# Performance work log

Hardware: AMD Instinct MI355X
Metric: run time of the kernel (lower is better)

Reference implementation:

```python
import jax, jax.numpy as jnp
import numpy as np

N = 65536      # points
C = 256        # channels
K = 16         # knn_samples
L = 4          # num_blocks
EXP = 4        # MLP expansion
EPS = 1e-5


def layer_norm(x, g, b):
    m = jnp.mean(x, axis=-1, keepdims=True)
    v = jnp.var(x, axis=-1, keepdims=True)
    return (x - m) * jax.lax.rsqrt(v + EPS) * g + b


def setup_inputs() -> dict:
    key = jax.random.key(0)
    ks = jax.random.split(key, 16)
    s = lambda fan_in: 1.0 / np.sqrt(fan_in)
    inp = {
        "x": jax.random.normal(ks[0], (N, C), jnp.float32),
        "knn_idx": jax.random.randint(ks[1], (N, K), 0, N, jnp.int32),
        # per-block stacked params (PyTorch Linear stored as [in, out] here)
        "ln1_g": jnp.ones((L, C), jnp.float32),
        "ln1_b": jnp.zeros((L, C), jnp.float32),
        "w_qkv": jax.random.uniform(ks[2], (L, C, 3 * C), jnp.float32, -s(C), s(C)),
        "w_proj": jax.random.uniform(ks[3], (L, C, C), jnp.float32, -s(C), s(C)),
        "b_proj": jax.random.uniform(ks[4], (L, C), jnp.float32, -s(C), s(C)),
        "ln2_g": jnp.ones((L, C), jnp.float32),
        "ln2_b": jnp.zeros((L, C), jnp.float32),
        "w_fc1": jax.random.uniform(ks[5], (L, C, EXP * C), jnp.float32, -s(C), s(C)),
        "b_fc1": jax.random.uniform(ks[6], (L, EXP * C), jnp.float32, -s(C), s(C)),
        "w_fc2": jax.random.uniform(ks[7], (L, EXP * C, C), jnp.float32, -s(EXP * C), s(EXP * C)),
        "b_fc2": jax.random.uniform(ks[8], (L, C), jnp.float32, -s(EXP * C), s(EXP * C)),
    }
    return inp


def reference(x, knn_idx, ln1_g, ln1_b, w_qkv, w_proj, b_proj,
              ln2_g, ln2_b, w_fc1, b_fc1, w_fc2, b_fc2):
    scale = C ** (-0.5)  # head_dim == C (num_heads == 1)
    for i in range(L):
        # --- KNN attention ---
        h = layer_norm(x, ln1_g[i], ln1_b[i])
        qkv = h @ w_qkv[i]                       # [N, 3C], no bias
        q, k, v = jnp.split(qkv, 3, axis=-1)     # each [N, C]
        kk = k[knn_idx]                          # [N, K, C] neighbor gather
        vv = v[knn_idx]                          # [N, K, C]
        scores = jnp.einsum('nc,nkc->nk', q, kk) * scale
        attn = jax.nn.softmax(scores, axis=-1)   # softmax over K neighbors
        out = jnp.einsum('nk,nkc->nc', attn, vv)
        x = x + (out @ w_proj[i] + b_proj[i])
        # --- MLP ---
        h2 = layer_norm(x, ln2_g[i], ln2_b[i])
        h2 = jax.nn.gelu(h2 @ w_fc1[i] + b_fc1[i], approximate=False)
        x = x + (h2 @ w_fc2[i] + b_fc2[i])
    return x
```

## Files before the change

### kernel.cpp

```cpp
#include <hip/hip_runtime.h>

typedef __attribute__((ext_vector_type(4))) float  f32x4;
typedef __attribute__((ext_vector_type(2))) float  f32x2;
typedef __attribute__((ext_vector_type(8))) __bf16 bf16x8;
typedef __attribute__((ext_vector_type(4))) short  s16x4;
typedef __attribute__((ext_vector_type(8))) short  s16x8;
typedef unsigned char uchar;

__device__ __forceinline__ unsigned short f2bf(float f) {
  unsigned u = __builtin_bit_cast(unsigned, f);
  u += 0x7FFFu + ((u >> 16) & 1u);
  return (unsigned short)(u >> 16);
}
__device__ __forceinline__ float b2f(short s) {
  return __builtin_bit_cast(float, (unsigned)((unsigned short)s) << 16);
}
__device__ __forceinline__ float gelu_sig(float v) {
  float t = __expf(-1.702f * v);
  return v * __builtin_amdgcn_rcpf(1.f + t);
}

__device__ __forceinline__ void gload16(const void* g, void* l) {
  __builtin_amdgcn_global_load_lds(
      (const __attribute__((address_space(1))) void*)g,
      (__attribute__((address_space(3))) void*)l, 16, 0, 0);
}

__global__ __launch_bounds__(256) void x2bf(const float* __restrict__ x,
                                            short* __restrict__ xb) {
  int i = blockIdx.x * 256 + threadIdx.x;
  float4 v = *(const float4*)(x + (size_t)i * 4);
  s16x4 o;
  o[0] = (short)f2bf(v.x);
  o[1] = (short)f2bf(v.y);
  o[2] = (short)f2bf(v.z);
  o[3] = (short)f2bf(v.w);
  *(s16x4*)(xb + (size_t)i * 4) = o;
}

__global__ __launch_bounds__(256) void wcast(const float* __restrict__ W,
                                             short* __restrict__ WT,
                                             int In, int Out) {
  int i = blockIdx.x * 256 + threadIdx.x;
  int lay = blockIdx.y;
  if (i >= In * Out) return;
  const float* w = W + (size_t)lay * In * Out;
  short* wt = WT + (size_t)lay * In * Out;
  int ii = i % In, oo = i / In;
  wt[(size_t)oo * In + ii] = (short)f2bf(w[(size_t)ii * Out + oo]);
}

__global__ __launch_bounds__(256) void ln_k(const short* __restrict__ xb,
                                            const float* __restrict__ g,
                                            const float* __restrict__ b,
                                            short* __restrict__ out) {
  int row = blockIdx.x * 4 + (threadIdx.x >> 6);
  int l = threadIdx.x & 63;
  const s16x4 vb = *(const s16x4*)(xb + (size_t)row * 256 + l * 4);
  float v0 = b2f(vb[0]), v1 = b2f(vb[1]), v2 = b2f(vb[2]), v3 = b2f(vb[3]);
  float s  = v0 + v1 + v2 + v3;
  float ss = v0 * v0 + v1 * v1 + v2 * v2 + v3 * v3;
#pragma unroll
  for (int o = 32; o >= 1; o >>= 1) {
    s  += __shfl_xor(s, o);
    ss += __shfl_xor(ss, o);
  }
  float mean = s * (1.0f / 256.0f);
  float var  = ss * (1.0f / 256.0f) - mean * mean;
  float rstd = rsqrtf(var + 1e-5f);
  const float4 gg = *(const float4*)(g + l * 4);
  const float4 bb = *(const float4*)(b + l * 4);
  s16x4 o4;
  o4[0] = (short)f2bf((v0 - mean) * rstd * gg.x + bb.x);
  o4[1] = (short)f2bf((v1 - mean) * rstd * gg.y + bb.y);
  o4[2] = (short)f2bf((v2 - mean) * rstd * gg.z + bb.z);
  o4[3] = (short)f2bf((v3 - mean) * rstd * gg.w + bb.w);
  *(s16x4*)(out + (size_t)row * 256 + l * 4) = o4;
}

__global__ __launch_bounds__(256) void attn_k(const short* __restrict__ q_,
                                              const uchar* __restrict__ k8,
                                              const uchar* __restrict__ v8,
                                              const int* __restrict__ knn,
                                              short* __restrict__ out) {
  int n = blockIdx.x * 4 + (threadIdx.x >> 6);
  int l = threadIdx.x & 63;
  int j = l & 15, g = l >> 4;
  int idxj = knn[(size_t)n * 16 + j];
  const short* qp = q_ + (size_t)n * 256 + g * 64;
  const uchar* kp = k8 + (size_t)idxj * 256 + g * 64;
  float partial = 0.f;
#pragma unroll
  for (int t = 0; t < 4; ++t) {
    int4 kv = *(const int4*)(kp + t * 16);
    s16x8 q0 = *(const s16x8*)(qp + t * 16);
    s16x8 q1 = *(const s16x8*)(qp + t * 16 + 8);
    f32x2 a;
    a = __builtin_amdgcn_cvt_pk_f32_fp8(kv.x, false);
    partial += a[0] * b2f(q0[0]) + a[1] * b2f(q0[1]);
    a = __builtin_amdgcn_cvt_pk_f32_fp8(kv.x, true);
    partial += a[0] * b2f(q0[2]) + a[1] * b2f(q0[3]);
    a = __builtin_amdgcn_cvt_pk_f32_fp8(kv.y, false);
    partial += a[0] * b2f(q0[4]) + a[1] * b2f(q0[5]);
    a = __builtin_amdgcn_cvt_pk_f32_fp8(kv.y, true);
    partial += a[0] * b2f(q0[6]) + a[1] * b2f(q0[7]);
    a = __builtin_amdgcn_cvt_pk_f32_fp8(kv.z, false);
    partial += a[0] * b2f(q1[0]) + a[1] * b2f(q1[1]);
    a = __builtin_amdgcn_cvt_pk_f32_fp8(kv.z, true);
    partial += a[0] * b2f(q1[2]) + a[1] * b2f(q1[3]);
    a = __builtin_amdgcn_cvt_pk_f32_fp8(kv.w, false);
    partial += a[0] * b2f(q1[4]) + a[1] * b2f(q1[5]);
    a = __builtin_amdgcn_cvt_pk_f32_fp8(kv.w, true);
    partial += a[0] * b2f(q1[6]) + a[1] * b2f(q1[7]);
  }
  partial += __shfl_xor(partial, 16);
  partial += __shfl_xor(partial, 32);
  float score = partial * 0.0625f;
  float mx = score;
#pragma unroll
  for (int o = 1; o < 16; o <<= 1) mx = fmaxf(mx, __shfl_xor(mx, o));
  float e = __expf(score - mx);
  float sum = e;
#pragma unroll
  for (int o = 1; o < 16; o <<= 1) sum += __shfl_xor(sum, o);
  float attn = e / sum;
  float4 o4 = {0.f, 0.f, 0.f, 0.f};
#pragma unroll
  for (int jj = 0; jj < 16; ++jj) {
    float aj = __shfl(attn, jj);
    int   ij = __shfl(idxj, jj);
    int vv = *(const int*)(v8 + (size_t)ij * 256 + l * 4);
    f32x2 lo = __builtin_amdgcn_cvt_pk_f32_fp8(vv, false);
    f32x2 hi = __builtin_amdgcn_cvt_pk_f32_fp8(vv, true);
    o4.x += aj * lo[0];
    o4.y += aj * lo[1];
    o4.z += aj * hi[0];
    o4.w += aj * hi[1];
  }
  s16x4 ob;
  ob[0] = (short)f2bf(o4.x);
  ob[1] = (short)f2bf(o4.y);
  ob[2] = (short)f2bf(o4.z);
  ob[3] = (short)f2bf(o4.w);
  *(s16x4*)(out + (size_t)n * 256 + l * 4) = ob;
}

template <int EPI, int KD>
__global__ __launch_bounds__(256) void gemm_k(
    const short* __restrict__ A, const short* __restrict__ BT,
    const float* __restrict__ bias, const short* __restrict__ residb,
    short* __restrict__ outb, float* __restrict__ outf,
    uchar* __restrict__ k8, uchar* __restrict__ v8, int Nout, int gx) {
  __shared__ __align__(16) char pool[36864];
  short* lA = (short*)pool;
  short* lB = (short*)(pool + 16384);
  const int tid = threadIdx.x;
  const int l = tid & 63, w = tid >> 6;
  const int nwg = gridDim.x;
  const int bid = blockIdx.x;
  const int swz = (bid & 7) * (nwg >> 3) + (bid >> 3);
  const int m0 = (swz / gx) << 7, n0 = (swz % gx) << 7;
  const int wm = w >> 1, wn = w & 1;

  f32x4 acc[4][4];
#pragma unroll
  for (int i = 0; i < 4; ++i)
#pragma unroll
    for (int jj = 0; jj < 4; ++jj) acc[i][jj] = f32x4{0.f, 0.f, 0.f, 0.f};

  const int srow = (w << 3) + (l >> 3);
  const int scol = (((l & 7) << 3)) ^ ((srow & 7) << 3);
  const short* gA = A + (size_t)(m0 + srow) * KD + scol;
  const short* gB = BT + (size_t)(n0 + srow) * KD + scol;

  for (int kt = 0; kt < KD; kt += 64) {
#pragma unroll
    for (int it = 0; it < 4; ++it) {
      gload16(gA + (size_t)(it * 32) * KD + kt, &lA[(it * 32 + w * 8) * 64]);
      gload16(gB + (size_t)(it * 32) * KD + kt, &lB[(it * 32 + w * 8) * 64]);
    }
    __syncthreads();
#pragma unroll
    for (int kc = 0; kc < 2; ++kc) {
      bf16x8 aF[4], bF[4];
#pragma unroll
      for (int f = 0; f < 4; ++f) {
        int r = wm * 64 + f * 16 + (l & 15);
        int ce = (kc * 32 + ((l >> 4) << 3)) ^ ((r & 7) << 3);
        aF[f] = *(const bf16x8*)(lA + r * 64 + ce);
      }
#pragma unroll
      for (int f = 0; f < 4; ++f) {
        int r = wn * 64 + f * 16 + (l & 15);
        int ce = (kc * 32 + ((l >> 4) << 3)) ^ ((r & 7) << 3);
        bF[f] = *(const bf16x8*)(lB + r * 64 + ce);
      }
#pragma unroll
      for (int mf = 0; mf < 4; ++mf)
#pragma unroll
        for (int nf = 0; nf < 4; ++nf)
          acc[mf][nf] = __builtin_amdgcn_mfma_f32_16x16x32_bf16(
              aF[mf], bF[nf], acc[mf][nf], 0, 0, 0);
    }
    __syncthreads();
  }

  const int lr = (l >> 4) << 2, lc = l & 15;
  if (EPI == 1 || EPI == 4) {
#pragma unroll
    for (int mf = 0; mf < 4; ++mf) {
#pragma unroll
      for (int nf = 0; nf < 4; ++nf) {
#pragma unroll
        for (int jj = 0; jj < 4; ++jj) {
          int row = m0 + wm * 64 + mf * 16 + lr + jj;
          int col = n0 + wn * 64 + nf * 16 + lc;
          float v = acc[mf][nf][jj] + bias[col] +
                    b2f(residb[(size_t)row * 256 + col]);
          if (EPI == 1)
            outb[(size_t)row * 256 + col] = (short)f2bf(v);
          else
            outf[(size_t)row * 256 + col] = v;
        }
      }
    }
    return;
  }

  short* myL = (short*)(pool + w * 9216);
#pragma unroll
  for (int mf = 0; mf < 4; ++mf) {
#pragma unroll
    for (int nf = 0; nf < 4; ++nf) {
#pragma unroll
      for (int jj = 0; jj < 4; ++jj) {
        int rl = mf * 16 + lr + jj;
        int cl = nf * 16 + lc;
        float v = acc[mf][nf][jj];
        if (EPI == 2) v = gelu_sig(v + bias[n0 + wn * 64 + cl]);
        myL[rl * 72 + cl] = (short)f2bf(v);
      }
    }
  }
#pragma unroll
  for (int it = 0; it < 8; ++it) {
    int rl = it * 8 + (l >> 3);
    int cl = (l & 7) * 8;
    s16x8 vv = *(const s16x8*)(myL + rl * 72 + cl);
    int rowg = m0 + wm * 64 + rl;
    int colg = n0 + wn * 64 + cl;
    if (EPI == 2) {
      *(s16x8*)(outb + (size_t)rowg * Nout + colg) = vv;
    } else {
      if (colg < 256) {
        *(s16x8*)(outb + (size_t)rowg * 256 + colg) = vv;
      } else {
        unsigned w0 = __builtin_amdgcn_cvt_pk_fp8_f32(b2f(vv[0]), b2f(vv[1]), 0, false);
        w0 = __builtin_amdgcn_cvt_pk_fp8_f32(b2f(vv[2]), b2f(vv[3]), w0, true);
        unsigned w1 = __builtin_amdgcn_cvt_pk_fp8_f32(b2f(vv[4]), b2f(vv[5]), 0, false);
        w1 = __builtin_amdgcn_cvt_pk_fp8_f32(b2f(vv[6]), b2f(vv[7]), w1, true);
        int2 pk = make_int2((int)w0, (int)w1);
        uchar* dst = (colg < 512) ? (k8 + (size_t)rowg * 256 + (colg - 256))
                                  : (v8 + (size_t)rowg * 256 + (colg - 512));
        *(int2*)dst = pk;
      }
    }
  }
}

extern "C" void kernel_launch(void* const* d_in, const int* in_sizes, int n_in,
                              void* d_out, int out_size, void* d_ws, size_t ws_size,
                              hipStream_t stream) {
  const float* in_x   = (const float*)d_in[0];
  const int*   knn    = (const int*)d_in[1];
  const float* ln1_g  = (const float*)d_in[2];
  const float* ln1_b  = (const float*)d_in[3];
  const float* w_qkv  = (const float*)d_in[4];
  const float* w_proj = (const float*)d_in[5];
  const float* b_proj = (const float*)d_in[6];
  const float* ln2_g  = (const float*)d_in[7];
  const float* ln2_b  = (const float*)d_in[8];
  const float* w_fc1  = (const float*)d_in[9];
  const float* b_fc1  = (const float*)d_in[10];
  const float* w_fc2  = (const float*)d_in[11];
  const float* b_fc2  = (const float*)d_in[12];

  char* ws = (char*)d_ws;
  short* xb   = (short*)(ws);
  short* act  = (short*)(ws + 33554432);
  short* big  = (short*)(ws + 67108864);
  short* q_bf = big;
  uchar* k8   = (uchar*)(ws + 100663296);
  uchar* v8   = (uchar*)(ws + 117440512);
  short* wT   = (short*)(ws + 201326592);
  short* wqkvT  = wT;
  short* wprojT = wT + 786432;
  short* wfc1T  = wT + 1048576;
  short* wfc2T  = wT + 2097152;

  x2bf<<<16384, 256, 0, stream>>>(in_x, xb);
  wcast<<<dim3(768, 4), 256, 0, stream>>>(w_qkv, wqkvT, 256, 768);
  wcast<<<dim3(256, 4), 256, 0, stream>>>(w_proj, wprojT, 256, 256);
  wcast<<<dim3(1024, 4), 256, 0, stream>>>(w_fc1, wfc1T, 256, 1024);
  wcast<<<dim3(1024, 4), 256, 0, stream>>>(w_fc2, wfc2T, 1024, 256);

  for (int i = 0; i < 4; ++i) {
    ln_k<<<16384, 256, 0, stream>>>(xb, ln1_g + i * 256, ln1_b + i * 256, act);
    gemm_k<3, 256><<<3072, 256, 0, stream>>>(
        act, wqkvT + (size_t)i * 196608, nullptr, nullptr, q_bf, nullptr,
        k8, v8, 768, 6);
    attn_k<<<16384, 256, 0, stream>>>(q_bf, k8, v8, knn, act);
    gemm_k<1, 256><<<1024, 256, 0, stream>>>(
        act, wprojT + (size_t)i * 65536, b_proj + i * 256, xb, xb,
        nullptr, nullptr, nullptr, 256, 2);
    ln_k<<<16384, 256, 0, stream>>>(xb, ln2_g + i * 256, ln2_b + i * 256, act);
    gemm_k<2, 256><<<4096, 256, 0, stream>>>(
        act, wfc1T + (size_t)i * 262144, b_fc1 + i * 1024, nullptr, big,
        nullptr, nullptr, nullptr, 1024, 8);
    if (i < 3)
      gemm_k<1, 1024><<<1024, 256, 0, stream>>>(
          big, wfc2T + (size_t)i * 262144, b_fc2 + i * 256, xb, xb,
          nullptr, nullptr, nullptr, 256, 2);
    else
      gemm_k<4, 1024><<<1024, 256, 0, stream>>>(
          big, wfc2T + (size_t)i * 262144, b_fc2 + i * 256, xb, nullptr,
          (float*)d_out, nullptr, nullptr, 256, 2);
  }
}
```

Before: 1.084 ms.

## Fuse LayerNorm into proj and fc2 GEMM epilogues with full-row tiles

Adds a gemm_ln kernel where each 512-thread workgroup computes a 128x256 tile covering the full channel width. It adds bias and residual, writes the bf16 residual stream, then reduces row sum and sum of squares across waves in shared memory to apply the next LayerNorm. This removes seven of the eight standalone ln_k launches and their extra read and write of the activation. The cost is fewer, larger workgroups (512 instead of 1024) and no double buffering in the new kernel. Variance now comes from E[x^2]-mean^2 on the bf16-rounded-before values rather than a separate pass.

```diff
diff --git a/kernel.cpp b/kernel.cpp
--- a/kernel.cpp
+++ b/kernel.cpp
@@ -206,7 +206,7 @@
   }
 
   const int lr = (l >> 4) << 2, lc = l & 15;
-  if (EPI == 1 || EPI == 4) {
+  if (EPI == 4) {
 #pragma unroll
     for (int mf = 0; mf < 4; ++mf) {
 #pragma unroll
@@ -217,10 +217,7 @@
           int col = n0 + wn * 64 + nf * 16 + lc;
           float v = acc[mf][nf][jj] + bias[col] +
                     b2f(residb[(size_t)row * 256 + col]);
-          if (EPI == 1)
-            outb[(size_t)row * 256 + col] = (short)f2bf(v);
-          else
-            outf[(size_t)row * 256 + col] = v;
+          outf[(size_t)row * 256 + col] = v;
         }
       }
     }
@@ -268,6 +265,118 @@
   }
 }
 
+template <int KD>
+__global__ __launch_bounds__(512) void gemm_ln(
+    const short* __restrict__ A, const short* __restrict__ BT,
+    const float* __restrict__ bias, const short* __restrict__ residb,
+    short* __restrict__ xbout, const float* __restrict__ lng,
+    const float* __restrict__ lnb, short* __restrict__ actout) {
+  __shared__ __align__(16) short lA[128 * 64];
+  __shared__ __align__(16) short lB[256 * 64];
+  __shared__ float psum[4][128], psq[4][128];
+  const int tid = threadIdx.x;
+  const int l = tid & 63, w = tid >> 6;
+  const int nwg = gridDim.x;
+  const int bid = blockIdx.x;
+  const int swz = (bid & 7) * (nwg >> 3) + (bid >> 3);
+  const int m0 = swz << 7;
+  const int wm = w >> 2, wn = w & 3;
+
+  f32x4 acc[4][4];
+#pragma unroll
+  for (int i = 0; i < 4; ++i)
+#pragma unroll
+    for (int jj = 0; jj < 4; ++jj) acc[i][jj] = f32x4{0.f, 0.f, 0.f, 0.f};
+
+  const int srow = (w << 3) + (l >> 3);
+  const int scol = (((l & 7) << 3)) ^ ((srow & 7) << 3);
+  const short* gA = A + (size_t)(m0 + srow) * KD + scol;
+  const short* gB = BT + (size_t)srow * KD + scol;
+
+  for (int kt = 0; kt < KD; kt += 64) {
+#pragma unroll
+    for (int it = 0; it < 2; ++it)
+      gload16(gA + (size_t)(it * 64) * KD + kt, &lA[(it * 64 + w * 8) * 64]);
+#pragma unroll
+    for (int it = 0; it < 4; ++it)
+      gload16(gB + (size_t)(it * 64) * KD + kt, &lB[(it * 64 + w * 8) * 64]);
+    __syncthreads();
+#pragma unroll
+    for (int kc = 0; kc < 2; ++kc) {
+      bf16x8 aF[4], bF[4];
+#pragma unroll
+      for (int f = 0; f < 4; ++f) {
+        int r = wm * 64 + f * 16 + (l & 15);
+        int ce = (kc * 32 + ((l >> 4) << 3)) ^ ((r & 7) << 3);
+        aF[f] = *(const bf16x8*)(lA + r * 64 + ce);
+      }
+#pragma unroll
+      for (int f = 0; f < 4; ++f) {
+        int r = wn * 64 + f * 16 + (l & 15);
+        int ce = (kc * 32 + ((l >> 4) << 3)) ^ ((r & 7) << 3);
+        bF[f] = *(const bf16x8*)(lB + r * 64 + ce);
+      }
+#pragma unroll
+      for (int mf = 0; mf < 4; ++mf)
+#pragma unroll
+        for (int nf = 0; nf < 4; ++nf)
+          acc[mf][nf] = __builtin_amdgcn_mfma_f32_16x16x32_bf16(
+              aF[mf], bF[nf], acc[mf][nf], 0, 0, 0);
+    }
+    __syncthreads();
+  }
+
+  const int lr = (l >> 4) << 2, lc = l & 15;
+#pragma unroll
+  for (int mf = 0; mf < 4; ++mf) {
+#pragma unroll
+    for (int jj = 0; jj < 4; ++jj) {
+      int rowl = wm * 64 + mf * 16 + lr + jj;
+      int row = m0 + rowl;
+      float s = 0.f, q = 0.f;
+#pragma unroll
+      for (int nf = 0; nf < 4; ++nf) {
+        int col = wn * 64 + nf * 16 + lc;
+        float v = acc[mf][nf][jj] + bias[col] +
+                  b2f(residb[(size_t)row * 256 + col]);
+        acc[mf][nf][jj] = v;
+        xbout[(size_t)row * 256 + col] = (short)f2bf(v);
+        s += v;
+        q += v * v;
+      }
+#pragma unroll
+      for (int off = 1; off < 16; off <<= 1) {
+        s += __shfl_xor(s, off);
+        q += __shfl_xor(q, off);
+      }
+      if (lc == 0) {
+        psum[wn][rowl] = s;
+        psq[wn][rowl] = q;
+      }
+    }
+  }
+  __syncthreads();
+#pragma unroll
+  for (int mf = 0; mf < 4; ++mf) {
+#pragma unroll
+    for (int jj = 0; jj < 4; ++jj) {
+      int rowl = wm * 64 + mf * 16 + lr + jj;
+      int row = m0 + rowl;
+      float S = psum[0][rowl] + psum[1][rowl] + psum[2][rowl] + psum[3][rowl];
+      float Q = psq[0][rowl] + psq[1][rowl] + psq[2][rowl] + psq[3][rowl];
+      float mean = S * (1.0f / 256.0f);
+      float var = Q * (1.0f / 256.0f) - mean * mean;
+      float rstd = rsqrtf(var + 1e-5f);
+#pragma unroll
+      for (int nf = 0; nf < 4; ++nf) {
+        int col = wn * 64 + nf * 16 + lc;
+        float v = (acc[mf][nf][jj] - mean) * rstd * lng[col] + lnb[col];
+        actout[(size_t)row * 256 + col] = (short)f2bf(v);
+      }
+    }
+  }
+}
+
 extern "C" void kernel_launch(void* const* d_in, const int* in_sizes, int n_in,
                               void* d_out, int out_size, void* d_ws, size_t ws_size,
                               hipStream_t stream) {
@@ -304,23 +413,23 @@
   wcast<<<dim3(1024, 4), 256, 0, stream>>>(w_fc1, wfc1T, 256, 1024);
   wcast<<<dim3(1024, 4), 256, 0, stream>>>(w_fc2, wfc2T, 1024, 256);
 
+  ln_k<<<16384, 256, 0, stream>>>(xb, ln1_g, ln1_b, act);
+
   for (int i = 0; i < 4; ++i) {
-    ln_k<<<16384, 256, 0, stream>>>(xb, ln1_g + i * 256, ln1_b + i * 256, act);
     gemm_k<3, 256><<<3072, 256, 0, stream>>>(
         act, wqkvT + (size_t)i * 196608, nullptr, nullptr, q_bf, nullptr,
         k8, v8, 768, 6);
     attn_k<<<16384, 256, 0, stream>>>(q_bf, k8, v8, knn, act);
-    gemm_k<1, 256><<<1024, 256, 0, stream>>>(
+    gemm_ln<256><<<512, 512, 0, stream>>>(
         act, wprojT + (size_t)i * 65536, b_proj + i * 256, xb, xb,
-        nullptr, nullptr, nullptr, 256, 2);
-    ln_k<<<16384, 256, 0, stream>>>(xb, ln2_g + i * 256, ln2_b + i * 256, act);
+        ln2_g + i * 256, ln2_b + i * 256, act);
     gemm_k<2, 256><<<4096, 256, 0, stream>>>(
         act, wfc1T + (size_t)i * 262144, b_fc1 + i * 1024, nullptr, big,
         nullptr, nullptr, nullptr, 1024, 8);
     if (i < 3)
-      gemm_k<1, 1024><<<1024, 256, 0, stream>>>(
+      gemm_ln<1024><<<512, 512, 0, stream>>>(
           big, wfc2T + (size_t)i * 262144, b_fc2 + i * 256, xb, xb,
-          nullptr, nullptr, nullptr, 256, 2);
+          ln1_g + (i + 1) * 256, ln1_b + (i + 1) * 256, act);
     else
       gemm_k<4, 1024><<<1024, 256, 0, stream>>>(
           big, wfc2T + (size_t)i * 262144, b_fc2 + i * 256, xb, nullptr,
```

After: 1.121 ms. +3.4%, slower.
